# Kernel tuning notes

Measured on AMD Instinct MI355X. Metric: run time of the kernel, lower is better.

## Reference

```python
import jax, jax.numpy as jnp
import numpy as np
from jax import lax

# Constants matching PostProcess(conf_thres=0.4, iou_thres=0.5, merge=False, agnostic=False)
CONF_THRES = 0.4
IOU_THRES = 0.5
MAX_WH = 4096.0   # per-class box offset (agnostic=False)
MAX_DET = 300     # hardcoded in module
MAX_NMS = 30000   # cap on NMS candidates (yolov5 convention); JAX needs static shapes
B, N, NC = 16, 25200, 80


def setup_inputs() -> dict:
    key = jax.random.key(0)
    u = jax.random.uniform(key, (B, N, 5 + NC), dtype=jnp.float32)
    # cx,cy in [0,640); w,h in [2,102); obj and class scores in [0,1)
    scale = jnp.concatenate([jnp.array([640.0, 640.0, 100.0, 100.0], jnp.float32),
                             jnp.ones((1 + NC,), jnp.float32)])
    shift = jnp.concatenate([jnp.array([0.0, 0.0, 2.0, 2.0], jnp.float32),
                             jnp.zeros((1 + NC,), jnp.float32)])
    prediction = u * scale + shift
    return {"prediction": prediction}


def _cxcywh_to_xyxy(x):
    cx, cy, w, h = x[..., 0], x[..., 1], x[..., 2], x[..., 3]
    return jnp.stack([cx - 0.5 * w, cy - 0.5 * h, cx + 0.5 * w, cy + 0.5 * h], axis=-1)


def _process_one(x):  # x: [N, 5+NC]
    obj = x[:, 4]
    cls_conf = x[:, 5:] * obj[:, None]          # x[:,5:] *= x[:,4:5]
    box = _cxcywh_to_xyxy(x[:, :4])             # [N, 4]
    # multi-label candidate mask: obj > conf AND class conf > conf (x[xc] then x[:,5:] > conf)
    cand = (obj[:, None] > CONF_THRES) & (cls_conf > CONF_THRES)   # [N, NC]
    flat = jnp.where(cand, cls_conf, 0.0).reshape(-1)              # [N*NC]
    top_scores, top_idx = lax.top_k(flat, MAX_NMS)                 # static-size candidate set
    bi = top_idx // NC                                             # box index i
    cj = (top_idx % NC).astype(jnp.float32)                        # class index j
    cand_boxes = box[bi]                                           # [M, 4]
    scores0 = jnp.where(top_scores > CONF_THRES, top_scores, 0.0)  # 0 marks invalid/suppressed
    off_boxes = cand_boxes + cj[:, None] * MAX_WH                  # per-class offset for NMS
    areas = (off_boxes[:, 2] - off_boxes[:, 0]) * (off_boxes[:, 3] - off_boxes[:, 1])
    idx_range = jnp.arange(MAX_NMS)

    def step(scores, _):
        # greedy NMS: pick best remaining, suppress IoU > thresh (torchvision semantics)
        idx = jnp.argmax(scores)
        s = scores[idx]
        keep = s > 0.0
        b = off_boxes[idx]
        lt = jnp.maximum(b[:2], off_boxes[:, :2])
        rb = jnp.minimum(b[2:], off_boxes[:, 2:])
        wh = jnp.clip(rb - lt, 0.0)
        inter = wh[:, 0] * wh[:, 1]
        iou = inter / (areas[idx] + areas - inter + 1e-9)
        suppress = (iou > IOU_THRES) | (idx_range == idx)
        return jnp.where(suppress, 0.0, scores), (idx, keep)

    _, (keep_idx, keep_flag) = lax.scan(step, scores0, None, length=MAX_DET)
    rows = jnp.concatenate([cand_boxes[keep_idx],
                            top_scores[keep_idx][:, None],
                            cj[keep_idx][:, None]], axis=1)        # [MAX_DET, 6] = xyxy, conf, cls
    return jnp.where(keep_flag[:, None], rows, 0.0)


def reference(prediction):
    # Padded fixed-shape analogue of torch.stack(output): [B, MAX_DET, 6], zero rows = no detection
    return jax.vmap(_process_one)(prediction)
```

## Files before the change

### kernel.cpp

```cpp
#include <hip/hip_runtime.h>
#include <stdint.h>

#define BATCH 16
#define NROW 25200
#define NCLS 80
#define ROWF 85
#define MAXDET 300
#define MAXNMS 30000u
#define NBIN 3072
#define BASEBITS 0x3EC00000u
#define CAP 32768u
#define BATCH_FLOATS 2142000

#define PREBIN 2048
#define NBUCK 1024
#define CANDCAP 131072u
#define TOPK 2048u
#define K2CAP 4096u

#define SORTCAP 1024
#define CH_SZ 128

#define TILE_ROWS 80
#define TILE_FLOATS 6800
#define RPB 400
#define SUBT 5
#define SBLK 63

#define SBLK_S 105
#define RPB_S 240
#define TROWS 48
#define SUBT_S 5
#define ST_F4 1020u
#define B_F4 535500u
#define BLK_F4 5100u
#define TOTAL_F4 8568000u
#define KMAXS 1536u

__device__ __forceinline__ bool iou_gt_half(float ax1, float ay1, float ax2, float ay2, float aa,
                                            float bx1, float by1, float bx2, float by2, float ba) {
    float ltx = fmaxf(ax1, bx1), lty = fmaxf(ay1, by1);
    float rbx = fminf(ax2, bx2), rby = fminf(ay2, by2);
    float wx = fmaxf(__fsub_rn(rbx, ltx), 0.0f);
    float wy = fmaxf(__fsub_rn(rby, lty), 0.0f);
    float inter = __fmul_rn(wx, wy);
    float den = __fadd_rn(__fsub_rn(__fadd_rn(aa, ba), inter), 1e-9f);
    float t = __fmul_rn(0.5f, den);
    if (!(inter > t)) return false;
    float tg = __fmul_rn(0.50000012f, den);
    if (inter >= tg) return true;
    return __fdiv_rn(inter, den) > 0.5f;
}

__device__ __forceinline__ unsigned bin_of_bits(unsigned bits) {
    unsigned v = (bits - BASEBITS) >> 12;
    if (v > (unsigned)(NBIN - 1)) v = NBIN - 1;
    return v;
}

__device__ __forceinline__ void gload_lds16(const float4* g, float* lds_base_wave_uniform) {
    __builtin_amdgcn_global_load_lds((const __attribute__((address_space(1))) void*)g,
                                     (__attribute__((address_space(3))) void*)lds_base_wave_uniform,
                                     16, 0, 0);
}

__device__ __forceinline__ void stage_tile(const float4* __restrict__ predf4,
                                           float* lds_rows, unsigned tile_f4_base,
                                           int wv, int lane) {
    unsigned c0 = (unsigned)(wv << 7);
    #pragma unroll
    for (int j = 0; j < 2; ++j) {
        unsigned cb = c0 + (unsigned)(j << 6);
        unsigned gi = tile_f4_base + cb + (unsigned)lane;
        if (gi > TOTAL_F4 - 1u) gi = TOTAL_F4 - 1u;
        gload_lds16(predf4 + gi, lds_rows + (size_t)cb * 4);
    }
}

__global__ __launch_bounds__(512) void k_stage(const float* __restrict__ pred,
                                               unsigned* __restrict__ hist2,
                                               unsigned* __restrict__ ccnt,
                                               unsigned long long* __restrict__ cand,
                                               unsigned* __restrict__ oflow,
                                               int staged) {
    if (!staged) return;
    __shared__ __align__(16) float rows[2 * 4096];
    __shared__ unsigned shist[NBUCK];
    __shared__ unsigned long long skey[KMAXS];
    __shared__ unsigned s_cnt, s_n, s_base;
    int bx = blockIdx.x;
    int b = bx / SBLK_S, blk = bx - b * SBLK_S;
    int t = threadIdx.x, lane = t & 63, wv = t >> 6;
    for (int i = t; i < NBUCK; i += 512) shist[i] = 0u;
    if (t == 0) s_cnt = 0u;

    const float4* predf4 = (const float4*)pred;
    unsigned tb0 = (unsigned)b * B_F4 + (unsigned)blk * BLK_F4;
    int rowbase = blk * RPB_S;

    stage_tile(predf4, rows, tb0, wv, lane);
    __syncthreads();

    for (int st = 0; st < SUBT_S; ++st) {
        int buf = st & 1;
        if (st + 1 < SUBT_S)
            stage_tile(predf4, rows + ((buf ^ 1) << 12), tb0 + (unsigned)(st + 1) * ST_F4, wv, lane);

        const float* rb = rows + (buf << 12);
        for (int r = wv; r < TROWS; r += 8) {
            float obj = rb[r * ROWF + 4];
            if (!(obj > 0.4f)) continue;
            unsigned grow = (unsigned)(rowbase + st * TROWS + r);
            {
                float s = __fmul_rn(rb[r * ROWF + 5 + lane], obj);
                if (s >= 0.75f) {
                    unsigned bits = __float_as_uint(s);
                    atomicAdd(&shist[bin_of_bits(bits) - PREBIN], 1u);
                    unsigned u = atomicAdd(&s_cnt, 1u);
                    unsigned flat = grow * (unsigned)NCLS + (unsigned)lane;
                    if (u < KMAXS)
                        skey[u] = ((unsigned long long)bits << 32) |
                                  (unsigned long long)(0xFFFFFFFFu - flat);
                    else oflow[b] = 1u;
                }
            }
            if (lane < 16) {
                float s = __fmul_rn(rb[r * ROWF + 69 + lane], obj);
                if (s >= 0.75f) {
                    unsigned bits = __float_as_uint(s);
                    atomicAdd(&shist[bin_of_bits(bits) - PREBIN], 1u);
                    unsigned u = atomicAdd(&s_cnt, 1u);
                    unsigned flat = grow * (unsigned)NCLS + (unsigned)(64 + lane);
                    if (u < KMAXS)
                        skey[u] = ((unsigned long long)bits << 32) |
                                  (unsigned long long)(0xFFFFFFFFu - flat);
                    else oflow[b] = 1u;
                }
            }
        }
        __syncthreads();
    }

    unsigned* gh = hist2 + (size_t)b * NBUCK;
    for (int i = t; i < NBUCK; i += 512) {
        unsigned v = shist[i];
        if (v) atomicAdd(&gh[i], v);
    }
    if (t == 0) {
        unsigned n = s_cnt;
        if (n > KMAXS) n = KMAXS;
        unsigned base = atomicAdd(&ccnt[b], n);
        if (base + n > CANDCAP) oflow[b] = 1u;
        s_n = n; s_base = base;
    }
    __syncthreads();
    unsigned n = s_n, base = s_base;
    if (base + n <= CANDCAP) {
        unsigned long long* cd = cand + (size_t)b * CANDCAP + base;
        for (unsigned k = t; k < n; k += 512) cd[k] = skey[k];
    }
}

__global__ __launch_bounds__(1024) void k_prep(const unsigned* __restrict__ hist2,
                                               const unsigned* __restrict__ ccnt,
                                               const unsigned* __restrict__ oflow,
                                               const unsigned long long* __restrict__ cand,
                                               unsigned* __restrict__ suf2,
                                               unsigned long long* __restrict__ keys2,
                                               int* __restrict__ meta,
                                               int staged) {
    __shared__ unsigned sS[NBUCK];
    __shared__ unsigned scur[NBUCK];
    __shared__ int s_cut, s_need, s_tot, s_T, s_valid;
    __shared__ unsigned s_bad, s_E;
    int b = blockIdx.x, t = threadIdx.x;
    unsigned h = hist2[(size_t)b * NBUCK + t];
    sS[t] = h;
    if (t == 0) { s_cut = -1; s_T = -1; s_bad = 0u; s_need = 0; s_tot = 0; s_E = 0u; }
    __syncthreads();
    if (h > (unsigned)SORTCAP) atomicOr(&s_bad, 1u);
    for (int off = 1; off < NBUCK; off <<= 1) {
        unsigned v = (t + off < NBUCK) ? sS[t + off] : 0u;
        __syncthreads();
        sS[t] += v;
        __syncthreads();
    }
    unsigned Sv = sS[t];
    unsigned Sn = (t + 1 < NBUCK) ? sS[t + 1] : 0u;
    if (Sv >= MAXNMS && Sn < MAXNMS) {
        s_cut = PREBIN + t; s_need = (int)(MAXNMS - Sn); s_tot = (int)Sv;
    }
    if (Sv >= TOPK && Sn < TOPK) { s_T = PREBIN + t; s_E = Sv; }
    unsigned* g2 = suf2 + (size_t)b * (NBUCK + 1);
    g2[t] = Sv;
    if (t == 0) g2[NBUCK] = 0u;
    scur[t] = Sn;
    __syncthreads();
    if (t == 0) {
        int valid = (staged && s_cut >= 0 && s_T >= 0 && s_bad == 0u &&
                     oflow[b] == 0u && ccnt[b] <= CANDCAP) ? 1 : 0;
        s_valid = valid;
        meta[b * 8 + 0] = valid ? s_cut : 0;
        meta[b * 8 + 1] = valid ? s_need : 0;
        meta[b * 8 + 2] = valid ? s_tot : 0;
        meta[b * 8 + 3] = valid;
        meta[b * 8 + 4] = valid ? s_T : 0;
        meta[b * 8 + 5] = valid ? (int)s_E : 0;
    }
    __syncthreads();
    if (s_valid) {
        int T = s_T;
        unsigned ccb = ccnt[b];
        const unsigned long long* cd = cand + (size_t)b * CANDCAP;
        unsigned long long* k2 = keys2 + (size_t)b * K2CAP;
        for (unsigned k = t; k < ccb; k += 1024) {
            unsigned long long key = cd[k];
            unsigned v = bin_of_bits((unsigned)(key >> 32));
            if ((int)v >= T) {
                unsigned pos = atomicAdd(&scur[v - PREBIN], 1u);
                if (pos < K2CAP) k2[pos] = key;
            }
        }
    }
}

__global__ __launch_bounds__(256) void k_hist_fb(const float* __restrict__ pred,
                                                 unsigned* __restrict__ hist,
                                                 const int* __restrict__ meta) {
    int bx = blockIdx.x;
    int b = bx / SBLK, blk = bx - b * SBLK;
    if (meta[b * 8 + 3]) return;
    __shared__ __align__(16) float rows[TILE_FLOATS];
    __shared__ unsigned shist[NBIN];
    int t = threadIdx.x, lane = t & 63, wv = t >> 6;
    for (int i = t; i < NBIN; i += 256) shist[i] = 0u;
    const float* pbase = pred + (size_t)b * BATCH_FLOATS + (size_t)blk * RPB * ROWF;
    for (int st = 0; st < SUBT; ++st) {
        __syncthreads();
        const float4* src = (const float4*)(pbase + (size_t)st * TILE_ROWS * ROWF);
        float4* dst = (float4*)rows;
        for (int i = t; i < TILE_FLOATS / 4; i += 256) dst[i] = src[i];
        __syncthreads();
        for (int r = wv; r < TILE_ROWS; r += 4) {
            float obj = rows[r * ROWF + 4];
            if (!(obj > 0.4f)) continue;
            for (int half = 0; half < 2; ++half) {
                int c = lane + (half << 6);
                if (c < NCLS) {
                    float s = __fmul_rn(rows[r * ROWF + 5 + c], obj);
                    if (s > 0.4f) atomicAdd(&shist[bin_of_bits(__float_as_uint(s))], 1u);
                }
            }
        }
    }
    __syncthreads();
    unsigned* gh = hist + (size_t)b * NBIN;
    for (int i = t; i < NBIN; i += 256) {
        unsigned v = shist[i];
        if (v) atomicAdd(&gh[i], v);
    }
}

__global__ __launch_bounds__(256) void k_scan_fb(const unsigned* __restrict__ hist,
                                                 unsigned* __restrict__ suf,
                                                 int* __restrict__ meta) {
    int b = blockIdx.x, t = threadIdx.x;
    if (meta[b * 8 + 3]) return;
    __shared__ unsigned sh[NBIN];
    __shared__ unsigned sS[NBIN];
    __shared__ unsigned cs[256];
    __shared__ int s_cut, s_need, s_tot;
    const unsigned* gh = hist + (size_t)b * NBIN;
    for (int i = t; i < NBIN; i += 256) sh[i] = gh[i];
    if (t == 0) { s_cut = 0; s_need = 0x7FFFFFFF; s_tot = 0; }
    __syncthreads();
    const int CHUNK = NBIN / 256;
    int base = t * CHUNK;
    unsigned tot = 0;
    for (int i = 0; i < CHUNK; ++i) tot += sh[base + i];
    cs[t] = tot;
    __syncthreads();
    for (int off = 1; off < 256; off <<= 1) {
        unsigned v = (t + off < 256) ? cs[t + off] : 0u;
        __syncthreads();
        cs[t] += v;
        __syncthreads();
    }
    unsigned after = (t + 1 < 256) ? cs[t + 1] : 0u;
    for (int i = CHUNK - 1; i >= 0; --i) {
        after += sh[base + i];
        sS[base + i] = after;
    }
    __syncthreads();
    unsigned* gs = suf + (size_t)b * (NBIN + 1);
    for (int i = t; i < NBIN; i += 256) gs[i] = sS[i];
    if (t == 0) gs[NBIN] = 0u;
    for (int i = 0; i < CHUNK; ++i) {
        int v = base + i;
        unsigned Sv = sS[v];
        unsigned Sn = (v + 1 < NBIN) ? sS[v + 1] : 0u;
        if (Sv >= MAXNMS && Sn < MAXNMS) {
            s_cut = v; s_need = (int)(MAXNMS - Sn); s_tot = (int)Sv;
        }
    }
    __syncthreads();
    if (t == 0) {
        int cut = s_cut, needv = s_need, totv = s_tot;
        if (sS[0] < MAXNMS) { cut = 0; needv = 0x7FFFFFFF; totv = (int)sS[0]; }
        meta[b * 8 + 0] = cut;
        meta[b * 8 + 1] = needv;
        meta[b * 8 + 2] = totv;
    }
}

__global__ __launch_bounds__(256) void k_scatter_fb(const float* __restrict__ pred,
                                                    const unsigned* __restrict__ suf,
                                                    const int* __restrict__ meta,
                                                    unsigned* __restrict__ cursor,
                                                    unsigned long long* __restrict__ keys) {
    int bx = blockIdx.x;
    int b = bx / SBLK, blk = bx - b * SBLK;
    if (meta[b * 8 + 3]) return;
    __shared__ __align__(16) float rows[TILE_FLOATS];
    int t = threadIdx.x, lane = t & 63, wv = t >> 6;
    int cutbin = meta[b * 8 + 0];
    const float* pbase = pred + (size_t)b * BATCH_FLOATS + (size_t)blk * RPB * ROWF;
    unsigned rowbase0 = (unsigned)(blk * RPB);
    const unsigned* gs = suf + (size_t)b * (NBIN + 1);
    unsigned* cur = cursor + (size_t)b * NBIN;
    unsigned long long* kb = keys + (size_t)b * CAP;
    for (int st = 0; st < SUBT; ++st) {
        __syncthreads();
        const float4* src = (const float4*)(pbase + (size_t)st * TILE_ROWS * ROWF);
        float4* dst = (float4*)rows;
        for (int i = t; i < TILE_FLOATS / 4; i += 256) dst[i] = src[i];
        __syncthreads();
        for (int r = wv; r < TILE_ROWS; r += 4) {
            float obj = rows[r * ROWF + 4];
            if (!(obj > 0.4f)) continue;
            unsigned grow = rowbase0 + (unsigned)(st * TILE_ROWS + r);
            for (int half = 0; half < 2; ++half) {
                int c = lane + (half << 6);
                if (c < NCLS) {
                    float s = __fmul_rn(rows[r * ROWF + 5 + c], obj);
                    if (s > 0.4f) {
                        unsigned bits = __float_as_uint(s);
                        unsigned bin = bin_of_bits(bits);
                        if ((int)bin >= cutbin) {
                            unsigned pos = gs[bin + 1] + atomicAdd(&cur[bin], 1u);
                            if (pos < CAP) {
                                unsigned flat = grow * (unsigned)NCLS + (unsigned)c;
                                kb[pos] = ((unsigned long long)bits << 32) |
                                          (unsigned long long)(0xFFFFFFFFu - flat);
                            }
                        }
                    }
                }
            }
        }
    }
}

__global__ __launch_bounds__(1024) void k_nms(const float* __restrict__ pred,
                                              const unsigned* __restrict__ suf,
                                              const unsigned* __restrict__ suf2,
                                              const int* __restrict__ meta,
                                              const unsigned* __restrict__ ccnt,
                                              const unsigned long long* __restrict__ keys,
                                              const unsigned long long* __restrict__ keys2,
                                              const unsigned long long* __restrict__ cand,
                                              float* __restrict__ out) {
    __shared__ unsigned sgsL[NBUCK + 1];
    __shared__ unsigned long long ktmp[SORTCAP];
    __shared__ unsigned long long skeys[SORTCAP];
    __shared__ unsigned maskW[CH_SZ][5];
    __shared__ unsigned sup0w[4];
    __shared__ float cbox[CH_SZ][9];
    __shared__ float kept[MAXDET][5];
    __shared__ int klist[MAXDET];
    __shared__ int s_nk, s_localk;
    __shared__ unsigned s_gc;

    int b = blockIdx.x;
    int tid = threadIdx.x;
    int lane = tid & 63, wv = tid >> 6;

    int cutbin = meta[b * 8 + 0];
    int needv  = meta[b * 8 + 1];
    unsigned total = (unsigned)meta[b * 8 + 2];
    int valid  = meta[b * 8 + 3];
    int Tbin   = meta[b * 8 + 4];
    unsigned E = valid ? (unsigned)meta[b * 8 + 5] : 0u;
    if (!valid && total > CAP) total = CAP;
    const unsigned* gs = suf + (size_t)b * (NBIN + 1);
    const unsigned* g2 = suf2 + (size_t)b * (NBUCK + 1);
    const unsigned long long* kb = keys + (size_t)b * CAP;
    const unsigned long long* k2 = keys2 + (size_t)b * K2CAP;
    const unsigned long long* cd = cand + (size_t)b * CANDCAP;
    unsigned ccb = valid ? ccnt[b] : 0u;
    if (ccb > CANDCAP) ccb = CANDCAP;
    const float* pb = pred + (size_t)b * BATCH_FLOATS;
    float* ob = out + (size_t)b * MAXDET * 6;

    if (valid) for (int i = tid; i < NBUCK + 1; i += 1024) sgsL[i] = g2[i];
    if (tid == 0) s_nk = 0;
    __syncthreads();

#define GSV(v) (valid ? sgsL[(v) - PREBIN] : gs[(v)])

    unsigned limit;
    if (needv == 0x7FFFFFFF) limit = total;
    else limit = GSV(cutbin + 1) + (unsigned)needv;
    if (limit > total) limit = total;

    unsigned p = 0;
    while (p < limit) {
        if (s_nk >= MAXDET) break;

        int lo = cutbin, hi = NBIN - 1, vs = NBIN - 1;
        while (lo <= hi) { int mid = (lo + hi) >> 1;
            if (GSV(mid) <= p + (unsigned)SORTCAP) { vs = mid; hi = mid - 1; } else lo = mid + 1; }
        unsigned gEnd = GSV(vs);
        bool phaseA = (!valid) || (p < E);
        if (valid && phaseA && gEnd > E) gEnd = E;
        if (gEnd > total) gEnd = total;
        if (gEnd <= p) { gEnd = p + (unsigned)SORTCAP; if (gEnd > total) gEnd = total; }
        unsigned G = gEnd - p;

        if (phaseA) {
            const unsigned long long* src = valid ? k2 : kb;
            unsigned myLo = 0, myHi = 0;
            unsigned long long raw = 0ULL;
            if (tid < (int)G) {
                unsigned idx = p + (unsigned)tid;
                int l2 = cutbin, h2 = NBIN - 1, v = cutbin;
                while (l2 <= h2) { int mid = (l2 + h2) >> 1;
                    if (GSV(mid) > idx) { v = mid; l2 = mid + 1; } else h2 = mid - 1; }
                unsigned bstart = GSV(v + 1);
                unsigned bend = GSV(v);
                raw = src[idx];
                myLo = (bstart > p) ? (bstart - p) : 0u;
                myHi = bend - p; if (myHi > G) myHi = G;
                ktmp[tid] = raw;
            }
            __syncthreads();
            if (tid < (int)G) {
                unsigned rank = 0;
                for (unsigned u = myLo; u < myHi; ++u) rank += (ktmp[u] > raw) ? 1u : 0u;
                skeys[myLo + rank] = raw;
            }
            __syncthreads();
        } else {
            int l0 = cutbin, h0 = NBIN - 1, w1 = cutbin;
            while (l0 <= h0) { int mid = (l0 + h0) >> 1;
                if (GSV(mid) > p) { w1 = mid; l0 = mid + 1; } else h0 = mid - 1; }
            if (tid == 0) s_gc = 0u;
            __syncthreads();
            for (unsigned k = tid; k < ccb; k += 1024) {
                unsigned long long key = cd[k];
                unsigned v = bin_of_bits((unsigned)(key >> 32));
                if ((int)v >= vs && (int)v <= w1) {
                    unsigned u = atomicAdd(&s_gc, 1u);
                    if (u < (unsigned)SORTCAP) ktmp[u] = key;
                }
            }
            __syncthreads();
            unsigned Gc = s_gc; if (Gc > (unsigned)SORTCAP) Gc = (unsigned)SORTCAP;
            if (tid < (int)Gc) {
                unsigned long long key = ktmp[tid];
                unsigned v = bin_of_bits((unsigned)(key >> 32));
                unsigned bstart = GSV(v + 1);
                unsigned rank = 0;
                for (unsigned u = 0; u < Gc; ++u) {
                    unsigned long long kk = ktmp[u];
                    unsigned vu = bin_of_bits((unsigned)(kk >> 32));
                    rank += (vu == v && kk > key) ? 1u : 0u;
                }
                skeys[(bstart - p) + rank] = key;
            }
            __syncthreads();
        }

        unsigned consumable = limit - p; if (consumable > G) consumable = G;

        for (unsigned c0 = 0; c0 < consumable; c0 += CH_SZ) {
            int nk0 = s_nk;
            if (nk0 >= MAXDET) break;
            int CH = (int)((consumable - c0 < (unsigned)CH_SZ) ? (consumable - c0) : (unsigned)CH_SZ);

            if (tid < CH_SZ * 5) maskW[tid / 5][tid % 5] = 0u;
            if (tid >= CH_SZ * 5 && tid < CH_SZ * 5 + 4) sup0w[tid - CH_SZ * 5] = 0u;
            if (tid < CH) {
                unsigned long long kk = skeys[c0 + tid];
                unsigned flat = 0xFFFFFFFFu - (unsigned)kk;
                unsigned bi = flat / (unsigned)NCLS;
                unsigned cc = flat - bi * (unsigned)NCLS;
                const float* rp = pb + (size_t)bi * ROWF;
                float cx = rp[0], cy = rp[1], wd = rp[2], ht = rp[3];
                float hw = __fmul_rn(0.5f, wd), hh = __fmul_rn(0.5f, ht);
                float off = __fmul_rn((float)cc, 4096.0f);
                float x1 = __fsub_rn(cx, hw), y1 = __fsub_rn(cy, hh);
                float x2 = __fadd_rn(cx, hw), y2 = __fadd_rn(cy, hh);
                float ox1 = __fadd_rn(x1, off), oy1 = __fadd_rn(y1, off);
                float ox2 = __fadd_rn(x2, off), oy2 = __fadd_rn(y2, off);
                cbox[tid][0] = ox1; cbox[tid][1] = oy1;
                cbox[tid][2] = ox2; cbox[tid][3] = oy2;
                cbox[tid][4] = __fmul_rn(__fsub_rn(ox2, ox1), __fsub_rn(oy2, oy1));
            }
            __syncthreads();

            {
                int col = tid & (CH_SZ - 1);
                int part = tid >> 7;
                if (col < CH) {
                    float bx1 = cbox[col][0], by1 = cbox[col][1];
                    float bx2 = cbox[col][2], by2 = cbox[col][3], ba = cbox[col][4];
                    unsigned part16 = 0u;
                    int rbase = part << 4;
                    for (int k = 0; k < 16; ++k) {
                        int i2 = rbase + k;
                        if (i2 >= col || i2 >= CH) break;
                        if (iou_gt_half(cbox[i2][0], cbox[i2][1], cbox[i2][2], cbox[i2][3],
                                        cbox[i2][4], bx1, by1, bx2, by2, ba))
                            part16 |= (1u << k);
                    }
                    if (part16)
                        atomicOr(&maskW[col][part >> 1], part16 << ((part & 1) << 4));
                    bool f = false;
                    for (int k2 = part; k2 < nk0; k2 += 8) {
                        if (iou_gt_half(kept[k2][0], kept[k2][1], kept[k2][2], kept[k2][3],
                                        kept[k2][4], bx1, by1, bx2, by2, ba)) f = true;
                    }
                    if (f) atomicOr(&sup0w[col >> 5], 1u << (col & 31));
                }
            }
            __syncthreads();

            if (wv == 0) {
                unsigned keptw = 0u;
                int nkv = nk0, lk = 0;
                unsigned pre0 = (lane < 4 && CH > 0) ? maskW[0][lane] : 0u;
                unsigned pre1 = (lane < 4 && CH > 1) ? maskW[1][lane] : 0u;
                for (int j = 0; j < CH && nkv < MAXDET; ++j) {
                    unsigned colw = pre0;
                    pre0 = pre1;
                    pre1 = (lane < 4 && (j + 2) < CH) ? maskW[j + 2][lane] : 0u;
                    bool hit = (keptw & colw) != 0u;
                    bool sup = __any(hit);
                    if ((sup0w[j >> 5] >> (j & 31)) & 1u) sup = true;
                    if (!sup) {
                        if (lane == (j >> 5)) keptw |= 1u << (j & 31);
                        if (lane == 0) klist[lk] = j;
                        lk++; nkv++;
                    }
                }
                if (lane == 0) { s_localk = lk; s_nk = nkv; }
            }
            __syncthreads();

            int lk = s_localk;
            for (int t2 = tid; t2 < lk; t2 += 1024) {
                int i = klist[t2];
                int oidx = nk0 + t2;
                kept[oidx][0] = cbox[i][0]; kept[oidx][1] = cbox[i][1];
                kept[oidx][2] = cbox[i][2]; kept[oidx][3] = cbox[i][3];
                kept[oidx][4] = cbox[i][4];
                unsigned long long kk = skeys[c0 + i];
                unsigned bits = (unsigned)(kk >> 32);
                unsigned flat = 0xFFFFFFFFu - (unsigned)kk;
                unsigned bi = flat / (unsigned)NCLS;
                unsigned cc = flat - bi * (unsigned)NCLS;
                const float* rp = pb + (size_t)bi * ROWF;
                float cx = rp[0], cy = rp[1], wd = rp[2], ht = rp[3];
                float hw = __fmul_rn(0.5f, wd), hh = __fmul_rn(0.5f, ht);
                float* orow = ob + (size_t)oidx * 6;
                orow[0] = __fsub_rn(cx, hw);
                orow[1] = __fsub_rn(cy, hh);
                orow[2] = __fadd_rn(cx, hw);
                orow[3] = __fadd_rn(cy, hh);
                orow[4] = __uint_as_float(bits);
                orow[5] = (float)cc;
            }
            __syncthreads();
        }
        p = gEnd;
    }
#undef GSV
}

extern "C" void kernel_launch(void* const* d_in, const int* in_sizes, int n_in,
                              void* d_out, int out_size, void* d_ws, size_t ws_size,
                              hipStream_t stream) {
    const float* pred = (const float*)d_in[0];
    float* outp = (float*)d_out;
    char* ws = (char*)d_ws;

    const size_t OFF_HIST  = 0;
    const size_t SZ_HIST   = (size_t)BATCH * NBIN * 4;
    const size_t OFF_CUR   = OFF_HIST + SZ_HIST;
    const size_t SZ_CUR    = (size_t)BATCH * NBIN * 4;
    const size_t OFF_H2    = OFF_CUR + SZ_CUR;
    const size_t SZ_H2     = (size_t)BATCH * NBUCK * 4;
    const size_t OFF_CCNT  = OFF_H2 + SZ_H2;
    const size_t SZ_CCNT   = (size_t)BATCH * 4;
    const size_t OFF_OFLW  = OFF_CCNT + SZ_CCNT;
    const size_t SZ_OFLW   = (size_t)BATCH * 4;
    const size_t OFF_META  = OFF_OFLW + SZ_OFLW;
    const size_t SZ_META   = (size_t)BATCH * 8 * 4;
    const size_t ZERO_SZ   = OFF_META + SZ_META;
    const size_t OFF_SUF   = ZERO_SZ;
    const size_t SZ_SUF    = (size_t)BATCH * (NBIN + 1) * 4;
    const size_t OFF_SUF2  = OFF_SUF + SZ_SUF;
    const size_t SZ_SUF2   = (size_t)BATCH * (NBUCK + 1) * 4;
    const size_t OFF_KEYS  = OFF_SUF2 + SZ_SUF2;
    const size_t SZ_KEYS   = (size_t)BATCH * CAP * 8;
    const size_t OFF_K2    = OFF_KEYS + SZ_KEYS;
    const size_t SZ_K2     = (size_t)BATCH * K2CAP * 8;
    const size_t OFF_CAND  = OFF_K2 + SZ_K2;
    const size_t SZ_CAND   = (size_t)BATCH * CANDCAP * 8;
    const size_t WS_NEEDED = OFF_CAND + SZ_CAND;

    int staged = (ws_size >= WS_NEEDED) ? 1 : 0;

    unsigned* hist             = (unsigned*)(ws + OFF_HIST);
    unsigned* cursor           = (unsigned*)(ws + OFF_CUR);
    unsigned* hist2            = (unsigned*)(ws + OFF_H2);
    unsigned* ccnt             = (unsigned*)(ws + OFF_CCNT);
    unsigned* oflow            = (unsigned*)(ws + OFF_OFLW);
    int* meta                  = (int*)(ws + OFF_META);
    unsigned* suf              = (unsigned*)(ws + OFF_SUF);
    unsigned* suf2             = (unsigned*)(ws + OFF_SUF2);
    unsigned long long* keys   = (unsigned long long*)(ws + OFF_KEYS);
    unsigned long long* keys2  = (unsigned long long*)(ws + OFF_K2);
    unsigned long long* cand   = (unsigned long long*)(ws + OFF_CAND);

    hipMemsetAsync(ws, 0, ZERO_SZ, stream);
    hipMemsetAsync(d_out, 0, (size_t)out_size * sizeof(float), stream);

    k_stage<<<dim3(BATCH * SBLK_S), dim3(512), 0, stream>>>(pred, hist2, ccnt, cand, oflow, staged);
    k_prep<<<dim3(BATCH), dim3(1024), 0, stream>>>(hist2, ccnt, oflow, cand, suf2, keys2, meta, staged);
    k_hist_fb<<<dim3(BATCH * SBLK), dim3(256), 0, stream>>>(pred, hist, meta);
    k_scan_fb<<<dim3(BATCH), dim3(256), 0, stream>>>(hist, suf, meta);
    k_scatter_fb<<<dim3(BATCH * SBLK), dim3(256), 0, stream>>>(pred, suf, meta, cursor, keys);
    k_nms<<<dim3(BATCH), dim3(1024), 0, stream>>>(pred, suf, suf2, meta, ccnt, keys, keys2, cand, outp);
}
```

Measured before the change: 321.5 us.

## Give each wave private double-buffered chunks with wave-aggregated atomics in k_stage

The staging kernel now gives each wave its own 12-row chunk, double-buffered in LDS with global_load_lds and synchronised per wave through s_waitcnt, instead of block-wide tiles behind __syncthreads. Candidate slot allocation uses one ballot-aggregated atomic per wave in place of one per lane, and the histogram packs two 16-bit counters per word to halve LDS use. The grid shrinks to 70 blocks per batch of 360 rows each. This removes block barriers and atomic contention, but the per-wave LDS handoff depends on vmcnt ordering, and the 16-bit counters could overflow if a bin gets more than 65535 hits.

Result: no change. 327.7 us (+1.9%).

```diff
diff --git a/kernel.cpp b/kernel.cpp
--- a/kernel.cpp
+++ b/kernel.cpp
@@ -27,13 +27,12 @@
 #define SUBT 5
 #define SBLK 63
 
-#define SBLK_S 105
-#define RPB_S 240
-#define TROWS 48
-#define SUBT_S 5
-#define ST_F4 1020u
+#define SBLK2 70
+#define RPB2 360
+#define CH2 30
+#define CH_F4 255u
+#define BLK2_F4 7650u
 #define B_F4 535500u
-#define BLK_F4 5100u
 #define TOTAL_F4 8568000u
 #define KMAXS 1536u
 
@@ -64,16 +63,13 @@
                                      16, 0, 0);
 }
 
-__device__ __forceinline__ void stage_tile(const float4* __restrict__ predf4,
-                                           float* lds_rows, unsigned tile_f4_base,
-                                           int wv, int lane) {
-    unsigned c0 = (unsigned)(wv << 7);
+__device__ __forceinline__ void issue_chunk(const float4* __restrict__ predf4,
+                                            float* wbuf, unsigned chunk_f4_base, int lane) {
     #pragma unroll
-    for (int j = 0; j < 2; ++j) {
-        unsigned cb = c0 + (unsigned)(j << 6);
-        unsigned gi = tile_f4_base + cb + (unsigned)lane;
+    for (int j = 0; j < 4; ++j) {
+        unsigned gi = chunk_f4_base + (unsigned)(j << 6) + (unsigned)lane;
         if (gi > TOTAL_F4 - 1u) gi = TOTAL_F4 - 1u;
-        gload_lds16(predf4 + gi, lds_rows + (size_t)cb * 4);
+        gload_lds16(predf4 + gi, wbuf + (size_t)(j << 8));
     }
 }
 
@@ -84,67 +80,96 @@
                                                unsigned* __restrict__ oflow,
                                                int staged) {
     if (!staged) return;
-    __shared__ __align__(16) float rows[2 * 4096];
-    __shared__ unsigned shist[NBUCK];
+    __shared__ __align__(16) float rows[8 * 2 * 1024];
+    __shared__ unsigned shist32[NBUCK / 2];
     __shared__ unsigned long long skey[KMAXS];
     __shared__ unsigned s_cnt, s_n, s_base;
     int bx = blockIdx.x;
-    int b = bx / SBLK_S, blk = bx - b * SBLK_S;
+    int b = bx / SBLK2, blk = bx - b * SBLK2;
     int t = threadIdx.x, lane = t & 63, wv = t >> 6;
-    for (int i = t; i < NBUCK; i += 512) shist[i] = 0u;
+    if (t < NBUCK / 2) shist32[t] = 0u;
     if (t == 0) s_cnt = 0u;
 
     const float4* predf4 = (const float4*)pred;
-    unsigned tb0 = (unsigned)b * B_F4 + (unsigned)blk * BLK_F4;
-    int rowbase = blk * RPB_S;
-
-    stage_tile(predf4, rows, tb0, wv, lane);
-    __syncthreads();
-
-    for (int st = 0; st < SUBT_S; ++st) {
-        int buf = st & 1;
-        if (st + 1 < SUBT_S)
-            stage_tile(predf4, rows + ((buf ^ 1) << 12), tb0 + (unsigned)(st + 1) * ST_F4, wv, lane);
-
-        const float* rb = rows + (buf << 12);
-        for (int r = wv; r < TROWS; r += 8) {
+    unsigned tb0 = (unsigned)b * B_F4 + (unsigned)blk * BLK2_F4;
+    int rowbase = blk * RPB2;
+    float* wbase = rows + (wv << 11);
+
+    issue_chunk(predf4, wbase, tb0 + (unsigned)wv * CH_F4, lane);
+    __syncthreads();
+
+    int buf = 0;
+    for (int c = wv; c < CH2; c += 8) {
+        int nc = c + 8;
+        if (nc < CH2)
+            issue_chunk(predf4, wbase + ((buf ^ 1) << 10), tb0 + (unsigned)nc * CH_F4, lane);
+
+        const float* rb = wbase + (buf << 10);
+        int growbase = rowbase + c * 12;
+        for (int r = 0; r < 12; ++r) {
             float obj = rb[r * ROWF + 4];
-            if (!(obj > 0.4f)) continue;
-            unsigned grow = (unsigned)(rowbase + st * TROWS + r);
-            {
-                float s = __fmul_rn(rb[r * ROWF + 5 + lane], obj);
-                if (s >= 0.75f) {
-                    unsigned bits = __float_as_uint(s);
-                    atomicAdd(&shist[bin_of_bits(bits) - PREBIN], 1u);
-                    unsigned u = atomicAdd(&s_cnt, 1u);
-                    unsigned flat = grow * (unsigned)NCLS + (unsigned)lane;
-                    if (u < KMAXS)
-                        skey[u] = ((unsigned long long)bits << 32) |
-                                  (unsigned long long)(0xFFFFFFFFu - flat);
-                    else oflow[b] = 1u;
-                }
-            }
-            if (lane < 16) {
-                float s = __fmul_rn(rb[r * ROWF + 69 + lane], obj);
-                if (s >= 0.75f) {
-                    unsigned bits = __float_as_uint(s);
-                    atomicAdd(&shist[bin_of_bits(bits) - PREBIN], 1u);
-                    unsigned u = atomicAdd(&s_cnt, 1u);
-                    unsigned flat = grow * (unsigned)NCLS + (unsigned)(64 + lane);
-                    if (u < KMAXS)
-                        skey[u] = ((unsigned long long)bits << 32) |
-                                  (unsigned long long)(0xFFFFFFFFu - flat);
-                    else oflow[b] = 1u;
-                }
-            }
-        }
-        __syncthreads();
-    }
+            bool live = (obj > 0.4f);
+            if (live) {
+                unsigned grow = (unsigned)(growbase + r);
+                float s0 = __fmul_rn(rb[r * ROWF + 5 + lane], obj);
+                bool h0 = (s0 >= 0.75f);
+                unsigned long long m0 = __ballot(h0);
+                if (m0) {
+                    unsigned base0 = 0;
+                    int lead = (int)__builtin_ctzll(m0);
+                    if (lane == lead) base0 = atomicAdd(&s_cnt, (unsigned)__popcll(m0));
+                    base0 = (unsigned)__shfl((int)base0, lead);
+                    if (h0) {
+                        unsigned bits = __float_as_uint(s0);
+                        unsigned bin = bin_of_bits(bits) - PREBIN;
+                        atomicAdd(&shist32[bin >> 1], 1u << ((bin & 1) << 4));
+                        unsigned u = base0 + (unsigned)__popcll(m0 & ((1ULL << lane) - 1ULL));
+                        unsigned flat = grow * (unsigned)NCLS + (unsigned)lane;
+                        if (u < KMAXS)
+                            skey[u] = ((unsigned long long)bits << 32) |
+                                      (unsigned long long)(0xFFFFFFFFu - flat);
+                        else oflow[b] = 1u;
+                    }
+                }
+                bool h1 = false; float s1 = 0.0f;
+                if (lane < 16) {
+                    s1 = __fmul_rn(rb[r * ROWF + 69 + lane], obj);
+                    h1 = (s1 >= 0.75f);
+                }
+                unsigned long long m1 = __ballot(h1);
+                if (m1) {
+                    unsigned base1 = 0;
+                    int lead = (int)__builtin_ctzll(m1);
+                    if (lane == lead) base1 = atomicAdd(&s_cnt, (unsigned)__popcll(m1));
+                    base1 = (unsigned)__shfl((int)base1, lead);
+                    if (h1) {
+                        unsigned bits = __float_as_uint(s1);
+                        unsigned bin = bin_of_bits(bits) - PREBIN;
+                        atomicAdd(&shist32[bin >> 1], 1u << ((bin & 1) << 4));
+                        unsigned u = base1 + (unsigned)__popcll(m1 & ((1ULL << lane) - 1ULL));
+                        unsigned flat = grow * (unsigned)NCLS + (unsigned)(64 + lane);
+                        if (u < KMAXS)
+                            skey[u] = ((unsigned long long)bits << 32) |
+                                      (unsigned long long)(0xFFFFFFFFu - flat);
+                        else oflow[b] = 1u;
+                    }
+                }
+            }
+        }
+        if (nc < CH2) {
+            asm volatile("s_waitcnt vmcnt(0)" ::: "memory");
+        }
+        buf ^= 1;
+    }
+
+    __syncthreads();
 
     unsigned* gh = hist2 + (size_t)b * NBUCK;
-    for (int i = t; i < NBUCK; i += 512) {
-        unsigned v = shist[i];
-        if (v) atomicAdd(&gh[i], v);
+    if (t < NBUCK / 2) {
+        unsigned w = shist32[t];
+        unsigned lo = w & 0xFFFFu, hi = w >> 16;
+        if (lo) atomicAdd(&gh[2 * t], lo);
+        if (hi) atomicAdd(&gh[2 * t + 1], hi);
     }
     if (t == 0) {
         unsigned n = s_cnt;
@@ -637,7 +662,7 @@
     hipMemsetAsync(ws, 0, ZERO_SZ, stream);
     hipMemsetAsync(d_out, 0, (size_t)out_size * sizeof(float), stream);
 
-    k_stage<<<dim3(BATCH * SBLK_S), dim3(512), 0, stream>>>(pred, hist2, ccnt, cand, oflow, staged);
+    k_stage<<<dim3(BATCH * SBLK2), dim3(512), 0, stream>>>(pred, hist2, ccnt, cand, oflow, staged);
     k_prep<<<dim3(BATCH), dim3(1024), 0, stream>>>(hist2, ccnt, oflow, cand, suf2, keys2, meta, staged);
     k_hist_fb<<<dim3(BATCH * SBLK), dim3(256), 0, stream>>>(pred, hist, meta);
     k_scan_fb<<<dim3(BATCH), dim3(256), 0, stream>>>(hist, suf, meta);
```
